# Performance work log

Hardware: AMD Instinct MI355X
Metric: run time of the kernel (lower is better)

Reference implementation:

```python
import jax, jax.numpy as jnp
import numpy as np

N = 20000        # nodes
E = 320000       # edges (avg degree 16)
F_IN = 256       # n_feat
HID = 64         # n_hid (per-head channels, layer 1)
HEADS = 8        # hard-coded n_head in GAT2
NCLS = 64        # n_classes
NEG_SLOPE = 0.2  # PyG GATv2Conv default leaky_relu slope
EPS = 1e-16      # PyG softmax denominator epsilon


def setup_inputs() -> dict:
    key = jax.random.key(0)
    ks = jax.random.split(key, 10)
    glorot = lambda k, shape: jax.random.normal(k, shape, jnp.float32) * (1.0 / np.sqrt(shape[0]))
    return {
        "x": jax.random.normal(ks[0], (N, F_IN), jnp.float32),
        "edge_index": jax.random.randint(ks[1], (2, E), 0, N, dtype=jnp.int32),
        # layer 1: GATv2Conv(F_IN -> HID, heads=HEADS, concat=True)
        "Wl1": glorot(ks[2], (F_IN, HEADS * HID)),
        "Wr1": glorot(ks[3], (F_IN, HEADS * HID)),
        "att1": glorot(ks[4], (HEADS, HID)),
        "b1": jnp.zeros((HEADS * HID,), jnp.float32),
        # layer 2: GATv2Conv(HEADS*HID -> NCLS, heads=1, concat=False)
        "Wl2": glorot(ks[5], (HEADS * HID, NCLS)),
        "Wr2": glorot(ks[6], (HEADS * HID, NCLS)),
        "att2": glorot(ks[7], (1, NCLS)),
        "b2": jnp.zeros((NCLS,), jnp.float32),
    }


def gatv2_layer(x, Wl, Wr, att, bias, src, dst, heads, concat):
    # x: [N, Fin]; Wl/Wr: [Fin, heads*C]; att: [heads, C]
    n = x.shape[0]
    c = att.shape[1]
    xl = (x @ Wl).reshape(n, heads, c)   # source-side projection
    xr = (x @ Wr).reshape(n, heads, c)   # target-side projection
    # per-edge GATv2 score: a^T leaky_relu(Wl x_j + Wr x_i)
    e = jax.nn.leaky_relu(xl[src] + xr[dst], NEG_SLOPE)      # [E, H, C]
    alpha = jnp.einsum('ehc,hc->eh', e, att)                 # [E, H]
    # segment softmax over incoming edges of each target node
    amax = jax.ops.segment_max(alpha, dst, num_segments=n)   # [N, H]
    amax = jnp.where(jnp.isfinite(amax), amax, 0.0)
    ex = jnp.exp(alpha - amax[dst])
    denom = jax.ops.segment_sum(ex, dst, num_segments=n)     # [N, H]
    w = ex / (denom[dst] + EPS)                              # [E, H]
    # weighted scatter-aggregate of source features
    out = jax.ops.segment_sum(xl[src] * w[:, :, None], dst, num_segments=n)  # [N, H, C]
    out = out.reshape(n, heads * c) if concat else out.mean(axis=1)
    return out + bias


def reference(x, edge_index, Wl1, Wr1, att1, b1, Wl2, Wr2, att2, b2):
    src, dst = edge_index[0], edge_index[1]
    h = gatv2_layer(x, Wl1, Wr1, att1, b1, src, dst, HEADS, True)   # [N, 512]
    h = jax.nn.elu(h)
    out = gatv2_layer(h, Wl2, Wr2, att2, b2, src, dst, 1, False)    # [N, 64]
    return out
```

## Files before the change

kernel.cpp:

```cpp
#include <hip/hip_runtime.h>
#include <hip/hip_bf16.h>

#define N_NODES 20000
#define N_EDGES 320000
#define F_IN 256
#define HID 64
#define HEADS 8
#define NCLS 64
#define D1 (HEADS * HID)
#define SCAN_BLOCKS ((N_NODES + 255) / 256)

typedef __attribute__((ext_vector_type(8))) short short8;
typedef __attribute__((ext_vector_type(4))) float floatx4;
typedef __attribute__((ext_vector_type(2))) float v2f;

__device__ __forceinline__ ushort f2bf(float f) {
    unsigned u = __float_as_uint(f);
    unsigned r = (u + 0x7fffu + ((u >> 16) & 1u)) >> 16;
    return (ushort)r;
}
__device__ __forceinline__ v2f unpack2(unsigned u) {
    v2f r;
    r.x = __uint_as_float(u << 16);
    r.y = __uint_as_float(u & 0xffff0000u);
    return r;
}
template <int CTRL>
__device__ __forceinline__ float dppadd(float x) {
    int y = __builtin_amdgcn_update_dpp(0, __float_as_int(x), CTRL, 0xF, 0xF, true);
    return x + __int_as_float(y);
}
__device__ __forceinline__ float rowsum8(float x) {
    x = dppadd<0xB1>(x);
    x = dppadd<0x4E>(x);
    x = dppadd<0x141>(x);
    return x;
}
__device__ __forceinline__ float rowsum16(float x) {
    x = dppadd<0xB1>(x);
    x = dppadd<0x4E>(x);
    x = dppadd<0x124>(x);
    x = dppadd<0x128>(x);
    return x;
}
__device__ __forceinline__ float rowsum32(float x) {
    x = rowsum16(x);
    float t = __int_as_float(__builtin_amdgcn_ds_swizzle(__float_as_int(x), 0x401F));
    return x + t;
}

#define PB_HIST 1250
#define PB_CONV 5000
#define PB_T1   512
#define PB_T2   128
#define PB_TOTAL (PB_HIST + PB_CONV + 2 * PB_T1 + 2 * PB_T2)
__global__ __launch_bounds__(256) void preprocess(
    const float* __restrict__ x, ushort* __restrict__ xbf,
    const float* __restrict__ Wl1, const float* __restrict__ Wr1,
    const float* __restrict__ Wl2, const float* __restrict__ Wr2,
    ushort* __restrict__ wt1, ushort* __restrict__ wt2,
    const int* __restrict__ dst, int* __restrict__ cnt) {
    int b = blockIdx.x, t = threadIdx.x;
    if (b < PB_HIST) {
        int i = b * 256 + t;
        if (i < N_EDGES) atomicAdd(&cnt[dst[i]], 1);
    } else if (b < PB_HIST + PB_CONV) {
        int i = (b - PB_HIST) * 256 + t;
        if (i < N_NODES * F_IN / 4) {
            float4 v = ((const float4*)x)[i];
            ushort4 o;
            o.x = f2bf(v.x); o.y = f2bf(v.y); o.z = f2bf(v.z); o.w = f2bf(v.w);
            ((ushort4*)xbf)[i] = o;
        }
    } else if (b < PB_HIST + PB_CONV + 2 * PB_T1) {
        int lb = b - PB_HIST - PB_CONV;
        const float* W = (lb < PB_T1) ? Wl1 : Wr1;
        ushort* Wt = wt1 + ((lb < PB_T1) ? 0 : D1 * F_IN);
        int i = (lb % PB_T1) * 256 + t;
        if (i < D1 * F_IN) {
            int n = i >> 8, k = i & 255;
            Wt[i] = f2bf(W[(size_t)k * D1 + n]);
        }
    } else {
        int lb = b - PB_HIST - PB_CONV - 2 * PB_T1;
        const float* W = (lb < PB_T2) ? Wl2 : Wr2;
        ushort* Wt = wt2 + ((lb < PB_T2) ? 0 : NCLS * D1);
        int i = (lb % PB_T2) * 256 + t;
        if (i < NCLS * D1) {
            int n = i >> 9, k = i & 511;
            Wt[i] = f2bf(W[(size_t)k * NCLS + n]);
        }
    }
}

__global__ __launch_bounds__(256) void scan_local(const int* __restrict__ cnt,
                                                  int* __restrict__ pscan,
                                                  int* __restrict__ bsum, int n) {
    int tid = threadIdx.x;
    int i = blockIdx.x * 256 + tid;
    int lane = tid & 63, wave = tid >> 6;
    int v = (i < n) ? cnt[i] : 0;
    int x = v;
    #pragma unroll
    for (int d = 1; d < 64; d <<= 1) {
        int y = __shfl_up(x, d);
        if (lane >= d) x += y;
    }
    __shared__ int wsum[4];
    if (lane == 63) wsum[wave] = x;
    __syncthreads();
    int woff = 0;
    for (int w2 = 0; w2 < wave; w2++) woff += wsum[w2];
    int incl = x + woff;
    if (i < n) pscan[i] = incl;
    if (tid == 255) bsum[blockIdx.x] = incl;
}

__global__ __launch_bounds__(256) void scan_finalize(const int* __restrict__ cnt,
                                                     const int* __restrict__ pscan,
                                                     const int* __restrict__ bsum,
                                                     int* __restrict__ row_ptr,
                                                     int* __restrict__ cursor, int n) {
    int t = threadIdx.x;
    int lane = t & 63, wave = t >> 6;
    int v = (t < SCAN_BLOCKS && t < blockIdx.x) ? bsum[t] : 0;
    #pragma unroll
    for (int mask = 1; mask < 64; mask <<= 1) v += __shfl_xor(v, mask);
    __shared__ int ws[4];
    __shared__ int soff;
    if (lane == 0) ws[wave] = v;
    __syncthreads();
    if (t == 0) soff = ws[0] + ws[1] + ws[2] + ws[3];
    __syncthreads();
    int i = blockIdx.x * 256 + t;
    if (i < n) {
        int incl = pscan[i] + soff;
        row_ptr[i + 1] = incl;
        cursor[i] = incl - cnt[i];
    }
    if (i == 0) row_ptr[0] = 0;
}

#define APAD 40
#define G1_NT 8
#define G1_MT ((N_NODES + 127) / 128)
#define G1_BLOCKS (G1_NT * G1_MT)
#define SC_BLOCKS (N_EDGES / 256)
__global__ __launch_bounds__(256) void gemm1_scatter(
    const ushort* __restrict__ A, const ushort* __restrict__ Bt,
    ushort* __restrict__ C,
    const int* __restrict__ src, const int* __restrict__ dst,
    int* __restrict__ cursor, int* __restrict__ csr_src) {
    if (blockIdx.x >= G1_BLOCKS) {
        int i = (blockIdx.x - G1_BLOCKS) * 256 + threadIdx.x;
        if (i < N_EDGES) {
            int d = dst[i];
            int pos = atomicAdd(&cursor[d], 1);
            csr_src[pos] = src[i];
        }
        return;
    }
    const int M = N_NODES, N = 2 * D1, K = F_IN;
    __shared__ ushort As[128 * APAD];
    __shared__ ushort Bs[128 * APAD];
    int tid = threadIdx.x;
    int rowBase = (blockIdx.x >> 3) * 128, colBase = (blockIdx.x & 7) * 128;
    int wave = tid >> 6, lane = tid & 63;
    int quad = lane >> 4, m16 = lane & 15;
    int rh = wave >> 1, chf = wave & 1;
    floatx4 acc[4][4];
    #pragma unroll
    for (int i = 0; i < 4; i++)
        #pragma unroll
        for (int j = 0; j < 4; j++) acc[i][j] = (floatx4){0.f, 0.f, 0.f, 0.f};

    for (int k0 = 0; k0 < K; k0 += 32) {
        #pragma unroll
        for (int i = 0; i < 2; i++) {
            int idx = i * 256 + tid;
            int r = idx >> 2, kq = (idx & 3) * 8;
            int grow = rowBase + r;
            uint4 v = make_uint4(0, 0, 0, 0);
            if (grow < M) v = *(const uint4*)(A + (size_t)grow * K + k0 + kq);
            *(uint4*)&As[r * APAD + kq] = v;
            uint4 w = *(const uint4*)(Bt + (size_t)(colBase + r) * K + k0 + kq);
            *(uint4*)&Bs[r * APAD + kq] = w;
        }
        __syncthreads();
        short8 af[4], bfr[4];
        #pragma unroll
        for (int i = 0; i < 4; i++)
            af[i] = *(short8*)&As[(rh * 64 + i * 16 + m16) * APAD + quad * 8];
        #pragma unroll
        for (int j = 0; j < 4; j++)
            bfr[j] = *(short8*)&Bs[(chf * 64 + j * 16 + m16) * APAD + quad * 8];
        #pragma unroll
        for (int i = 0; i < 4; i++)
            #pragma unroll
            for (int j = 0; j < 4; j++)
                acc[i][j] = __builtin_amdgcn_mfma_f32_16x16x32_bf16(af[i], bfr[j], acc[i][j], 0, 0, 0);
        __syncthreads();
    }
    #pragma unroll
    for (int i = 0; i < 4; i++)
        #pragma unroll
        for (int j = 0; j < 4; j++)
            #pragma unroll
            for (int r = 0; r < 4; r++) {
                int row = rowBase + rh * 64 + i * 16 + quad * 4 + r;
                if (row < M) C[(size_t)row * N + colBase + chf * 64 + j * 16 + m16] = f2bf(acc[i][j][r]);
            }
}

__global__ __launch_bounds__(256) void gemm2_32x128(
    const ushort* __restrict__ A, const ushort* __restrict__ Bt,
    ushort* __restrict__ C) {
    const int K = D1;
    __shared__ ushort As[32 * APAD];
    __shared__ ushort Bs[128 * APAD];
    int tid = threadIdx.x;
    int rowBase = blockIdx.x * 32;
    int wave = tid >> 6, lane = tid & 63;
    int quad = lane >> 4, m16 = lane & 15;
    floatx4 acc[2][2];
    #pragma unroll
    for (int i = 0; i < 2; i++)
        #pragma unroll
        for (int j = 0; j < 2; j++) acc[i][j] = (floatx4){0.f, 0.f, 0.f, 0.f};

    for (int k0 = 0; k0 < K; k0 += 32) {
        if (tid < 128) {
            int r = tid >> 2, kq = (tid & 3) * 8;
            uint4 v = *(const uint4*)(A + (size_t)(rowBase + r) * K + k0 + kq);
            *(uint4*)&As[r * APAD + kq] = v;
        }
        #pragma unroll
        for (int i = 0; i < 2; i++) {
            int idx = i * 256 + tid;
            int r = idx >> 2, kq = (idx & 3) * 8;
            uint4 v = *(const uint4*)(Bt + (size_t)r * K + k0 + kq);
            *(uint4*)&Bs[r * APAD + kq] = v;
        }
        __syncthreads();
        short8 af[2], bfr[2];
        #pragma unroll
        for (int i = 0; i < 2; i++)
            af[i] = *(short8*)&As[(i * 16 + m16) * APAD + quad * 8];
        #pragma unroll
        for (int j = 0; j < 2; j++)
            bfr[j] = *(short8*)&Bs[(wave * 32 + j * 16 + m16) * APAD + quad * 8];
        #pragma unroll
        for (int i = 0; i < 2; i++)
            #pragma unroll
            for (int j = 0; j < 2; j++)
                acc[i][j] = __builtin_amdgcn_mfma_f32_16x16x32_bf16(af[i], bfr[j], acc[i][j], 0, 0, 0);
        __syncthreads();
    }
    #pragma unroll
    for (int i = 0; i < 2; i++)
        #pragma unroll
        for (int j = 0; j < 2; j++)
            #pragma unroll
            for (int r = 0; r < 4; r++) {
                int row = rowBase + i * 16 + quad * 4 + r;
                C[(size_t)row * 128 + wave * 32 + j * 16 + m16] = f2bf(acc[i][j][r]);
            }
}

#define L1PROC(cu, valid)                                                     \
    {                                                                         \
        v2f _c01 = unpack2((cu).x), _c23 = unpack2((cu).y);                   \
        v2f _c45 = unpack2((cu).z), _c67 = unpack2((cu).w);                   \
        v2f _v01 = _c01 + xr01, _v23 = _c23 + xr23;                           \
        v2f _v45 = _c45 + xr45, _v67 = _c67 + xr67;                           \
        v2f _sp = a6_01 * _v01 + a4_01 * __builtin_elementwise_abs(_v01);     \
        _sp = _sp + a6_23 * _v23 + a4_23 * __builtin_elementwise_abs(_v23);   \
        _sp = _sp + a6_45 * _v45 + a4_45 * __builtin_elementwise_abs(_v45);   \
        _sp = _sp + a6_67 * _v67 + a4_67 * __builtin_elementwise_abs(_v67);   \
        float _sc = _sp.x + _sp.y;                                            \
        _sc = rowsum8(_sc);                                                   \
        float _e = (valid) ? exp2f(_sc) : 0.f;                                \
        den += _e;                                                            \
        v2f _ev = {_e, _e};                                                   \
        ac01 = ac01 + _ev * _c01; ac23 = ac23 + _ev * _c23;                   \
        ac45 = ac45 + _ev * _c45; ac67 = ac67 + _ev * _c67;                   \
    }

__global__ __launch_bounds__(128) void attn_l1_fused(
    const ushort* __restrict__ xlr, const float* __restrict__ att,
    const float* __restrict__ b1,
    const int* __restrict__ row_ptr, const int* __restrict__ csr_src,
    ushort* __restrict__ h1out) {
    int d = blockIdx.x;
    int wave = threadIdx.x >> 6, lane = threadIdx.x & 63;
    int start = row_ptr[d], deg = row_ptr[d + 1] - start;

    uint4 xru = *(const uint4*)(xlr + (size_t)d * 1024 + 512 + 8 * lane);
    v2f xr01 = unpack2(xru.x), xr23 = unpack2(xru.y);
    v2f xr45 = unpack2(xru.z), xr67 = unpack2(xru.w);
    const float C6 = 0.6f * 1.44269504f, C4 = 0.4f * 1.44269504f;
    float4 atA = *(const float4*)(att + 8 * lane);
    float4 atB = *(const float4*)(att + 8 * lane + 4);
    v2f a6_01 = {C6 * atA.x, C6 * atA.y}, a4_01 = {C4 * atA.x, C4 * atA.y};
    v2f a6_23 = {C6 * atA.z, C6 * atA.w}, a4_23 = {C4 * atA.z, C4 * atA.w};
    v2f a6_45 = {C6 * atB.x, C6 * atB.y}, a4_45 = {C4 * atB.x, C4 * atB.y};
    v2f a6_67 = {C6 * atB.z, C6 * atB.w}, a4_67 = {C4 * atB.z, C4 * atB.w};

    float den = 0.f;
    v2f ac01 = {0.f, 0.f}, ac23 = {0.f, 0.f}, ac45 = {0.f, 0.f}, ac67 = {0.f, 0.f};

    int S = (deg > wave) ? ((deg - wave + 1) >> 1) : 0;
    if (S > 0) {
        const int* cs = csr_src + start + wave;
        uint4 q0 = *(const uint4*)(xlr + (size_t)cs[0] * 1024 + 8 * lane);
        uint4 q1 = *(const uint4*)(xlr + (size_t)cs[2 * min(1, S - 1)] * 1024 + 8 * lane);
        uint4 q2 = *(const uint4*)(xlr + (size_t)cs[2 * min(2, S - 1)] * 1024 + 8 * lane);
        uint4 q3 = *(const uint4*)(xlr + (size_t)cs[2 * min(3, S - 1)] * 1024 + 8 * lane);
        for (int i0 = 0; i0 < S; i0 += 4) {
            uint4 e0 = q0, e1 = q1, e2 = q2, e3 = q3;
            if (i0 + 4 < S) q0 = *(const uint4*)(xlr + (size_t)cs[2 * (i0 + 4)] * 1024 + 8 * lane);
            if (i0 + 5 < S) q1 = *(const uint4*)(xlr + (size_t)cs[2 * (i0 + 5)] * 1024 + 8 * lane);
            if (i0 + 6 < S) q2 = *(const uint4*)(xlr + (size_t)cs[2 * (i0 + 6)] * 1024 + 8 * lane);
            if (i0 + 7 < S) q3 = *(const uint4*)(xlr + (size_t)cs[2 * (i0 + 7)] * 1024 + 8 * lane);
            L1PROC(e0, true)
            L1PROC(e1, i0 + 1 < S)
            L1PROC(e2, i0 + 2 < S)
            L1PROC(e3, i0 + 3 < S)
        }
    }
    __shared__ float sden2[64];
    __shared__ float sacc[64][10];
    if (wave == 1) {
        sden2[lane] = den;
        float4 f0 = {ac01.x, ac01.y, ac23.x, ac23.y};
        float4 f1 = {ac45.x, ac45.y, ac67.x, ac67.y};
        *(float4*)&sacc[lane][0] = f0;
        *(float4*)&sacc[lane][4] = f1;
    }
    __syncthreads();
    if (wave == 0) {
        den += sden2[lane];
        float4 g0 = *(float4*)&sacc[lane][0];
        float4 g1 = *(float4*)&sacc[lane][4];
        float inv = 1.f / (den + 1e-16f);
        float4 bA = *(const float4*)(b1 + 8 * lane);
        float4 bB = *(const float4*)(b1 + 8 * lane + 4);
        float o0 = (ac01.x + g0.x) * inv + bA.x;
        float o1 = (ac01.y + g0.y) * inv + bA.y;
        float o2 = (ac23.x + g0.z) * inv + bA.z;
        float o3 = (ac23.y + g0.w) * inv + bA.w;
        float o4 = (ac45.x + g1.x) * inv + bB.x;
        float o5 = (ac45.y + g1.y) * inv + bB.y;
        float o6 = (ac67.x + g1.z) * inv + bB.z;
        float o7 = (ac67.y + g1.w) * inv + bB.w;
        o0 = o0 > 0.f ? o0 : (__expf(o0) - 1.f);
        o1 = o1 > 0.f ? o1 : (__expf(o1) - 1.f);
        o2 = o2 > 0.f ? o2 : (__expf(o2) - 1.f);
        o3 = o3 > 0.f ? o3 : (__expf(o3) - 1.f);
        o4 = o4 > 0.f ? o4 : (__expf(o4) - 1.f);
        o5 = o5 > 0.f ? o5 : (__expf(o5) - 1.f);
        o6 = o6 > 0.f ? o6 : (__expf(o6) - 1.f);
        o7 = o7 > 0.f ? o7 : (__expf(o7) - 1.f);
        ushort4 h0, h1v;
        h0.x = f2bf(o0); h0.y = f2bf(o1); h0.z = f2bf(o2); h0.w = f2bf(o3);
        h1v.x = f2bf(o4); h1v.y = f2bf(o5); h1v.z = f2bf(o6); h1v.w = f2bf(o7);
        *(ushort4*)(h1out + (size_t)d * D1 + 8 * lane) = h0;
        *(ushort4*)(h1out + (size_t)d * D1 + 8 * lane + 4) = h1v;
    }
}

#define L2PROC(cu, valid)                                                     \
    {                                                                         \
        v2f _cv = unpack2(cu);                                                \
        v2f _vv = _cv + yr2;                                                  \
        v2f _spv = at6 * _vv + at4 * __builtin_elementwise_abs(_vv);          \
        float _sc = _spv.x + _spv.y;                                          \
        _sc = rowsum32(_sc);                                                  \
        float _e = (valid) ? exp2f(_sc) : 0.f;                                \
        den += _e;                                                            \
        v2f _ev = {_e, _e};                                                   \
        acc = acc + _ev * _cv;                                                \
    }

__global__ __launch_bounds__(256) void attn_l2_fused(
    const ushort* __restrict__ ylr, const float* __restrict__ att2,
    const float* __restrict__ b2,
    const int* __restrict__ row_ptr, const int* __restrict__ csr_src,
    float* __restrict__ out) {
    int wave = threadIdx.x >> 6, lane = threadIdx.x & 63;
    int d = blockIdx.x * 4 + wave;
    if (d >= N_NODES) return;
    int half = lane >> 5, l31 = lane & 31;
    int start = row_ptr[d], deg = row_ptr[d + 1] - start;

    unsigned yru = *(const unsigned*)(ylr + (size_t)d * 128 + 64 + 2 * l31);
    v2f yr2 = unpack2(yru);
    float2 a2 = *(const float2*)(att2 + 2 * l31);
    const float C6 = 0.6f * 1.44269504f, C4 = 0.4f * 1.44269504f;
    v2f at6 = {C6 * a2.x, C6 * a2.y};
    v2f at4 = {C4 * a2.x, C4 * a2.y};

    float den = 0.f;
    v2f acc = {0.f, 0.f};

    if (deg > 0) {
        int S = (deg + 1) >> 1;
        const int* cs = csr_src + start;
        int p0i = min(0 + half, deg - 1);
        int p1i = min(2 * min(1, S - 1) + half, deg - 1);
        int p2i = min(2 * min(2, S - 1) + half, deg - 1);
        int p3i = min(2 * min(3, S - 1) + half, deg - 1);
        unsigned y0 = *(const unsigned*)(ylr + (size_t)cs[p0i] * 128 + 2 * l31);
        unsigned y1 = *(const unsigned*)(ylr + (size_t)cs[p1i] * 128 + 2 * l31);
        unsigned y2 = *(const unsigned*)(ylr + (size_t)cs[p2i] * 128 + 2 * l31);
        unsigned y3 = *(const unsigned*)(ylr + (size_t)cs[p3i] * 128 + 2 * l31);
        for (int i0 = 0; i0 < S; i0 += 4) {
            unsigned u0 = y0, u1 = y1, u2 = y2, u3 = y3;
            if (i0 + 4 < S) { int p = min(2 * (i0 + 4) + half, deg - 1); y0 = *(const unsigned*)(ylr + (size_t)cs[p] * 128 + 2 * l31); }
            if (i0 + 5 < S) { int p = min(2 * (i0 + 5) + half, deg - 1); y1 = *(const unsigned*)(ylr + (size_t)cs[p] * 128 + 2 * l31); }
            if (i0 + 6 < S) { int p = min(2 * (i0 + 6) + half, deg - 1); y2 = *(const unsigned*)(ylr + (size_t)cs[p] * 128 + 2 * l31); }
            if (i0 + 7 < S) { int p = min(2 * (i0 + 7) + half, deg - 1); y3 = *(const unsigned*)(ylr + (size_t)cs[p] * 128 + 2 * l31); }
            L2PROC(u0, 2 * (i0 + 0) + half < deg)
            L2PROC(u1, 2 * (i0 + 1) + half < deg)
            L2PROC(u2, 2 * (i0 + 2) + half < deg)
            L2PROC(u3, 2 * (i0 + 3) + half < deg)
        }
        den += __shfl_xor(den, 32);
        acc.x += __shfl_xor(acc.x, 32);
        acc.y += __shfl_xor(acc.y, 32);
    }
    if (half == 0) {
        float inv = 1.f / (den + 1e-16f);
        float2 bv = *(const float2*)(b2 + 2 * l31);
        float2 o;
        o.x = acc.x * inv + bv.x;
        o.y = acc.y * inv + bv.y;
        *(float2*)(out + (size_t)d * NCLS + 2 * l31) = o;
    }
}

extern "C" void kernel_launch(void* const* d_in, const int* in_sizes, int n_in,
                              void* d_out, int out_size, void* d_ws, size_t ws_size,
                              hipStream_t stream) {
    const float* x    = (const float*)d_in[0];
    const int*   edge = (const int*)d_in[1];
    const float* Wl1  = (const float*)d_in[2];
    const float* Wr1  = (const float*)d_in[3];
    const float* att1 = (const float*)d_in[4];
    const float* b1   = (const float*)d_in[5];
    const float* Wl2  = (const float*)d_in[6];
    const float* Wr2  = (const float*)d_in[7];
    const float* att2 = (const float*)d_in[8];
    const float* b2   = (const float*)d_in[9];
    float* out = (float*)d_out;

    const int* srcv = edge;
    const int* dstv = edge + N_EDGES;

    ushort* xbf  = (ushort*)d_ws;
    ushort* wt1  = xbf + (size_t)N_NODES * F_IN;
    ushort* wt2  = wt1 + 2 * D1 * F_IN;
    ushort* xlr  = wt2 + 2 * NCLS * D1;
    ushort* h1   = xlr + (size_t)N_NODES * 2 * D1;
    ushort* ylr  = h1 + (size_t)N_NODES * D1;
    int* cnt     = (int*)(ylr + (size_t)N_NODES * 2 * NCLS);
    int* pscan   = cnt + N_NODES;
    int* bsum    = pscan + N_NODES;
    int* row_ptr = bsum + 128;
    int* cursor  = row_ptr + N_NODES + 1;
    int* csr_src = cursor + N_NODES;

    hipMemsetAsync(cnt, 0, N_NODES * sizeof(int), stream);
    preprocess<<<PB_TOTAL, 256, 0, stream>>>(x, xbf, Wl1, Wr1, Wl2, Wr2, wt1, wt2, dstv, cnt);
    scan_local<<<SCAN_BLOCKS, 256, 0, stream>>>(cnt, pscan, bsum, N_NODES);
    scan_finalize<<<SCAN_BLOCKS, 256, 0, stream>>>(cnt, pscan, bsum, row_ptr, cursor, N_NODES);
    gemm1_scatter<<<G1_BLOCKS + SC_BLOCKS, 256, 0, stream>>>(
        xbf, wt1, xlr, srcv, dstv, cursor, csr_src);
    attn_l1_fused<<<N_NODES, 128, 0, stream>>>(xlr, att1, b1, row_ptr, csr_src, h1);
    gemm2_32x128<<<N_NODES / 32, 256, 0, stream>>>(h1, wt2, ylr);
    attn_l2_fused<<<(N_NODES + 3) / 4, 256, 0, stream>>>(ylr, att2, b2, row_ptr, csr_src, out);
}
```

Baseline: 227.1 us.

## Use async global-to-LDS loads in GEMMs and remap attention work per wave

Both GEMMs now stage tiles with global_load_lds direct-to-LDS copies into an unpadded 32-wide layout, replacing register round-trips and the padded layout. Layer-1 attention assigns one wave per node, removing the two-wave edge split and its LDS reduction and barrier. Layer-2 attention processes four edges per wave in 16-lane groups with 4 channels per lane, ending in a cross-group reduction. The trade-offs are possible LDS bank conflicts from dropping padding, and less memory-level parallelism per node in layer 1.

```diff
diff --git a/kernel.cpp b/kernel.cpp
--- a/kernel.cpp
+++ b/kernel.cpp
@@ -43,10 +43,10 @@
     x = dppadd<0x128>(x);
     return x;
 }
-__device__ __forceinline__ float rowsum32(float x) {
-    x = rowsum16(x);
-    float t = __int_as_float(__builtin_amdgcn_ds_swizzle(__float_as_int(x), 0x401F));
-    return x + t;
+__device__ __forceinline__ void async_copy16(ushort* lds, const ushort* g) {
+    __builtin_amdgcn_global_load_lds(
+        (const __attribute__((address_space(1))) void*)g,
+        (__attribute__((address_space(3))) void*)lds, 16, 0, 0);
 }
 
 #define PB_HIST 1250
@@ -141,7 +141,6 @@
     if (i == 0) row_ptr[0] = 0;
 }
 
-#define APAD 40
 #define G1_NT 8
 #define G1_MT ((N_NODES + 127) / 128)
 #define G1_BLOCKS (G1_NT * G1_MT)
@@ -161,8 +160,8 @@
         return;
     }
     const int M = N_NODES, N = 2 * D1, K = F_IN;
-    __shared__ ushort As[128 * APAD];
-    __shared__ ushort Bs[128 * APAD];
+    __shared__ ushort As[128 * 32];
+    __shared__ ushort Bs[128 * 32];
     int tid = threadIdx.x;
     int rowBase = (blockIdx.x >> 3) * 128, colBase = (blockIdx.x & 7) * 128;
     int wave = tid >> 6, lane = tid & 63;
@@ -179,21 +178,18 @@
         for (int i = 0; i < 2; i++) {
             int idx = i * 256 + tid;
             int r = idx >> 2, kq = (idx & 3) * 8;
-            int grow = rowBase + r;
-            uint4 v = make_uint4(0, 0, 0, 0);
-            if (grow < M) v = *(const uint4*)(A + (size_t)grow * K + k0 + kq);
-            *(uint4*)&As[r * APAD + kq] = v;
-            uint4 w = *(const uint4*)(Bt + (size_t)(colBase + r) * K + k0 + kq);
-            *(uint4*)&Bs[r * APAD + kq] = w;
+            int grow = min(rowBase + r, M - 1);
+            async_copy16(&As[idx * 8], A + (size_t)grow * K + k0 + kq);
+            async_copy16(&Bs[idx * 8], Bt + (size_t)(colBase + r) * K + k0 + kq);
         }
         __syncthreads();
         short8 af[4], bfr[4];
         #pragma unroll
         for (int i = 0; i < 4; i++)
-            af[i] = *(short8*)&As[(rh * 64 + i * 16 + m16) * APAD + quad * 8];
+            af[i] = *(short8*)&As[(rh * 64 + i * 16 + m16) * 32 + quad * 8];
         #pragma unroll
         for (int j = 0; j < 4; j++)
-            bfr[j] = *(short8*)&Bs[(chf * 64 + j * 16 + m16) * APAD + quad * 8];
+            bfr[j] = *(short8*)&Bs[(chf * 64 + j * 16 + m16) * 32 + quad * 8];
         #pragma unroll
         for (int i = 0; i < 4; i++)
             #pragma unroll
@@ -216,8 +212,8 @@
     const ushort* __restrict__ A, const ushort* __restrict__ Bt,
     ushort* __restrict__ C) {
     const int K = D1;
-    __shared__ ushort As[32 * APAD];
-    __shared__ ushort Bs[128 * APAD];
+    __shared__ ushort As[32 * 32];
+    __shared__ ushort Bs[128 * 32];
     int tid = threadIdx.x;
     int rowBase = blockIdx.x * 32;
     int wave = tid >> 6, lane = tid & 63;
@@ -231,24 +227,22 @@
     for (int k0 = 0; k0 < K; k0 += 32) {
         if (tid < 128) {
             int r = tid >> 2, kq = (tid & 3) * 8;
-            uint4 v = *(const uint4*)(A + (size_t)(rowBase + r) * K + k0 + kq);
-            *(uint4*)&As[r * APAD + kq] = v;
+            async_copy16(&As[tid * 8], A + (size_t)(rowBase + r) * K + k0 + kq);
         }
         #pragma unroll
         for (int i = 0; i < 2; i++) {
             int idx = i * 256 + tid;
             int r = idx >> 2, kq = (idx & 3) * 8;
-            uint4 v = *(const uint4*)(Bt + (size_t)r * K + k0 + kq);
-            *(uint4*)&Bs[r * APAD + kq] = v;
+            async_copy16(&Bs[idx * 8], Bt + (size_t)r * K + k0 + kq);
         }
         __syncthreads();
         short8 af[2], bfr[2];
         #pragma unroll
         for (int i = 0; i < 2; i++)
-            af[i] = *(short8*)&As[(i * 16 + m16) * APAD + quad * 8];
+            af[i] = *(short8*)&As[(i * 16 + m16) * 32 + quad * 8];
         #pragma unroll
         for (int j = 0; j < 2; j++)
-            bfr[j] = *(short8*)&Bs[(wave * 32 + j * 16 + m16) * APAD + quad * 8];
+            bfr[j] = *(short8*)&Bs[(wave * 32 + j * 16 + m16) * 32 + quad * 8];
         #pragma unroll
         for (int i = 0; i < 2; i++)
             #pragma unroll
@@ -286,13 +280,13 @@
         ac45 = ac45 + _ev * _c45; ac67 = ac67 + _ev * _c67;                   \
     }
 
-__global__ __launch_bounds__(128) void attn_l1_fused(
+__global__ __launch_bounds__(256) void attn_l1_fused(
     const ushort* __restrict__ xlr, const float* __restrict__ att,
     const float* __restrict__ b1,
     const int* __restrict__ row_ptr, const int* __restrict__ csr_src,
     ushort* __restrict__ h1out) {
-    int d = blockIdx.x;
     int wave = threadIdx.x >> 6, lane = threadIdx.x & 63;
+    int d = blockIdx.x * 4 + wave;
     int start = row_ptr[d], deg = row_ptr[d + 1] - start;
 
     uint4 xru = *(const uint4*)(xlr + (size_t)d * 1024 + 512 + 8 * lane);
@@ -309,78 +303,70 @@
     float den = 0.f;
     v2f ac01 = {0.f, 0.f}, ac23 = {0.f, 0.f}, ac45 = {0.f, 0.f}, ac67 = {0.f, 0.f};
 
-    int S = (deg > wave) ? ((deg - wave + 1) >> 1) : 0;
-    if (S > 0) {
-        const int* cs = csr_src + start + wave;
+    if (deg > 0) {
+        const int* cs = csr_src + start;
         uint4 q0 = *(const uint4*)(xlr + (size_t)cs[0] * 1024 + 8 * lane);
-        uint4 q1 = *(const uint4*)(xlr + (size_t)cs[2 * min(1, S - 1)] * 1024 + 8 * lane);
-        uint4 q2 = *(const uint4*)(xlr + (size_t)cs[2 * min(2, S - 1)] * 1024 + 8 * lane);
-        uint4 q3 = *(const uint4*)(xlr + (size_t)cs[2 * min(3, S - 1)] * 1024 + 8 * lane);
-        for (int i0 = 0; i0 < S; i0 += 4) {
+        uint4 q1 = *(const uint4*)(xlr + (size_t)cs[min(1, deg - 1)] * 1024 + 8 * lane);
+        uint4 q2 = *(const uint4*)(xlr + (size_t)cs[min(2, deg - 1)] * 1024 + 8 * lane);
+        uint4 q3 = *(const uint4*)(xlr + (size_t)cs[min(3, deg - 1)] * 1024 + 8 * lane);
+        for (int i0 = 0; i0 < deg; i0 += 4) {
             uint4 e0 = q0, e1 = q1, e2 = q2, e3 = q3;
-            if (i0 + 4 < S) q0 = *(const uint4*)(xlr + (size_t)cs[2 * (i0 + 4)] * 1024 + 8 * lane);
-            if (i0 + 5 < S) q1 = *(const uint4*)(xlr + (size_t)cs[2 * (i0 + 5)] * 1024 + 8 * lane);
-            if (i0 + 6 < S) q2 = *(const uint4*)(xlr + (size_t)cs[2 * (i0 + 6)] * 1024 + 8 * lane);
-            if (i0 + 7 < S) q3 = *(const uint4*)(xlr + (size_t)cs[2 * (i0 + 7)] * 1024 + 8 * lane);
+            if (i0 + 4 < deg) q0 = *(const uint4*)(xlr + (size_t)cs[i0 + 4] * 1024 + 8 * lane);
+            if (i0 + 5 < deg) q1 = *(const uint4*)(xlr + (size_t)cs[i0 + 5] * 1024 + 8 * lane);
+            if (i0 + 6 < deg) q2 = *(const uint4*)(xlr + (size_t)cs[i0 + 6] * 1024 + 8 * lane);
+            if (i0 + 7 < deg) q3 = *(const uint4*)(xlr + (size_t)cs[i0 + 7] * 1024 + 8 * lane);
             L1PROC(e0, true)
-            L1PROC(e1, i0 + 1 < S)
-            L1PROC(e2, i0 + 2 < S)
-            L1PROC(e3, i0 + 3 < S)
-        }
-    }
-    __shared__ float sden2[64];
-    __shared__ float sacc[64][10];
-    if (wave == 1) {
-        sden2[lane] = den;
-        float4 f0 = {ac01.x, ac01.y, ac23.x, ac23.y};
-        float4 f1 = {ac45.x, ac45.y, ac67.x, ac67.y};
-        *(float4*)&sacc[lane][0] = f0;
-        *(float4*)&sacc[lane][4] = f1;
-    }
-    __syncthreads();
-    if (wave == 0) {
-        den += sden2[lane];
-        float4 g0 = *(float4*)&sacc[lane][0];
-        float4 g1 = *(float4*)&sacc[lane][4];
-        float inv = 1.f / (den + 1e-16f);
-        float4 bA = *(const float4*)(b1 + 8 * lane);
-        float4 bB = *(const float4*)(b1 + 8 * lane + 4);
-        float o0 = (ac01.x + g0.x) * inv + bA.x;
-        float o1 = (ac01.y + g0.y) * inv + bA.y;
-        float o2 = (ac23.x + g0.z) * inv + bA.z;
-        float o3 = (ac23.y + g0.w) * inv + bA.w;
-        float o4 = (ac45.x + g1.x) * inv + bB.x;
-        float o5 = (ac45.y + g1.y) * inv + bB.y;
-        float o6 = (ac67.x + g1.z) * inv + bB.z;
-        float o7 = (ac67.y + g1.w) * inv + bB.w;
-        o0 = o0 > 0.f ? o0 : (__expf(o0) - 1.f);
-        o1 = o1 > 0.f ? o1 : (__expf(o1) - 1.f);
-        o2 = o2 > 0.f ? o2 : (__expf(o2) - 1.f);
-        o3 = o3 > 0.f ? o3 : (__expf(o3) - 1.f);
-        o4 = o4 > 0.f ? o4 : (__expf(o4) - 1.f);
-        o5 = o5 > 0.f ? o5 : (__expf(o5) - 1.f);
-        o6 = o6 > 0.f ? o6 : (__expf(o6) - 1.f);
-        o7 = o7 > 0.f ? o7 : (__expf(o7) - 1.f);
-        ushort4 h0, h1v;
-        h0.x = f2bf(o0); h0.y = f2bf(o1); h0.z = f2bf(o2); h0.w = f2bf(o3);
-        h1v.x = f2bf(o4); h1v.y = f2bf(o5); h1v.z = f2bf(o6); h1v.w = f2bf(o7);
-        *(ushort4*)(h1out + (size_t)d * D1 + 8 * lane) = h0;
-        *(ushort4*)(h1out + (size_t)d * D1 + 8 * lane + 4) = h1v;
-    }
+            L1PROC(e1, i0 + 1 < deg)
+            L1PROC(e2, i0 + 2 < deg)
+            L1PROC(e3, i0 + 3 < deg)
+        }
+    }
+    float inv = 1.f / (den + 1e-16f);
+    float4 bA = *(const float4*)(b1 + 8 * lane);
+    float4 bB = *(const float4*)(b1 + 8 * lane + 4);
+    float o0 = ac01.x * inv + bA.x;
+    float o1 = ac01.y * inv + bA.y;
+    float o2 = ac23.x * inv + bA.z;
+    float o3 = ac23.y * inv + bA.w;
+    float o4 = ac45.x * inv + bB.x;
+    float o5 = ac45.y * inv + bB.y;
+    float o6 = ac67.x * inv + bB.z;
+    float o7 = ac67.y * inv + bB.w;
+    o0 = o0 > 0.f ? o0 : (__expf(o0) - 1.f);
+    o1 = o1 > 0.f ? o1 : (__expf(o1) - 1.f);
+    o2 = o2 > 0.f ? o2 : (__expf(o2) - 1.f);
+    o3 = o3 > 0.f ? o3 : (__expf(o3) - 1.f);
+    o4 = o4 > 0.f ? o4 : (__expf(o4) - 1.f);
+    o5 = o5 > 0.f ? o5 : (__expf(o5) - 1.f);
+    o6 = o6 > 0.f ? o6 : (__expf(o6) - 1.f);
+    o7 = o7 > 0.f ? o7 : (__expf(o7) - 1.f);
+    ushort4 h0, h1v;
+    h0.x = f2bf(o0); h0.y = f2bf(o1); h0.z = f2bf(o2); h0.w = f2bf(o3);
+    h1v.x = f2bf(o4); h1v.y = f2bf(o5); h1v.z = f2bf(o6); h1v.w = f2bf(o7);
+    *(ushort4*)(h1out + (size_t)d * D1 + 8 * lane) = h0;
+    *(ushort4*)(h1out + (size_t)d * D1 + 8 * lane + 4) = h1v;
 }
 
 #define L2PROC(cu, valid)                                                     \
     {                                                                         \
-        v2f _cv = unpack2(cu);                                                \
-        v2f _vv = _cv + yr2;                                                  \
-        v2f _spv = at6 * _vv + at4 * __builtin_elementwise_abs(_vv);          \
-        float _sc = _spv.x + _spv.y;                                          \
-        _sc = rowsum32(_sc);                                                  \
+        v2f _c01 = unpack2((cu).x), _c23 = unpack2((cu).y);                   \
+        v2f _v01 = _c01 + yr01, _v23 = _c23 + yr23;                           \
+        v2f _sp = at6_01 * _v01 + at4_01 * __builtin_elementwise_abs(_v01)    \
+                + at6_23 * _v23 + at4_23 * __builtin_elementwise_abs(_v23);   \
+        float _sc = _sp.x + _sp.y;                                            \
+        _sc = rowsum16(_sc);                                                  \
         float _e = (valid) ? exp2f(_sc) : 0.f;                                \
         den += _e;                                                            \
         v2f _ev = {_e, _e};                                                   \
-        acc = acc + _ev * _cv;                                                \
-    }
+        ac01 = ac01 + _ev * _c01; ac23 = ac23 + _ev * _c23;                   \
+    }
+
+__device__ __forceinline__ float xgroup_sum(float x) {
+    float t = __int_as_float(__builtin_amdgcn_ds_swizzle(__float_as_int(x), 0x401F));
+    x += t;
+    x += __shfl_xor(x, 32);
+    return x;
+}
 
 __global__ __launch_bounds__(256) void attn_l2_fused(
     const ushort* __restrict__ ylr, const float* __restrict__ att2,
@@ -389,53 +375,48 @@
     float* __restrict__ out) {
     int wave = threadIdx.x >> 6, lane = threadIdx.x & 63;
     int d = blockIdx.x * 4 + wave;
-    if (d >= N_NODES) return;
-    int half = lane >> 5, l31 = lane & 31;
+    int grp = lane >> 4, l15 = lane & 15;
     int start = row_ptr[d], deg = row_ptr[d + 1] - start;
 
-    unsigned yru = *(const unsigned*)(ylr + (size_t)d * 128 + 64 + 2 * l31);
-    v2f yr2 = unpack2(yru);
-    float2 a2 = *(const float2*)(att2 + 2 * l31);
+    uint2 yru = *(const uint2*)(ylr + (size_t)d * 128 + 64 + 4 * l15);
+    v2f yr01 = unpack2(yru.x), yr23 = unpack2(yru.y);
+    float4 a2 = *(const float4*)(att2 + 4 * l15);
     const float C6 = 0.6f * 1.44269504f, C4 = 0.4f * 1.44269504f;
-    v2f at6 = {C6 * a2.x, C6 * a2.y};
-    v2f at4 = {C4 * a2.x, C4 * a2.y};
+    v2f at6_01 = {C6 * a2.x, C6 * a2.y}, at4_01 = {C4 * a2.x, C4 * a2.y};
+    v2f at6_23 = {C6 * a2.z, C6 * a2.w}, at4_23 = {C4 * a2.z, C4 * a2.w};
 
     float den = 0.f;
-    v2f acc = {0.f, 0.f};
+    v2f ac01 = {0.f, 0.f}, ac23 = {0.f, 0.f};
 
     if (deg > 0) {
-        int S = (deg + 1) >> 1;
+        int S = (deg + 3) >> 2;
         const int* cs = csr_src + start;
-        int p0i = min(0 + half, deg - 1);
-        int p1i = min(2 * min(1, S - 1) + half, deg - 1);
-        int p2i = min(2 * min(2, S - 1) + half, deg - 1);
-        int p3i = min(2 * min(3, S - 1) + half, deg - 1);
-        unsigned y0 = *(const unsigned*)(ylr + (size_t)cs[p0i] * 128 + 2 * l31);
-        unsigned y1 = *(const unsigned*)(ylr + (size_t)cs[p1i] * 128 + 2 * l31);
-        unsigned y2 = *(const unsigned*)(ylr + (size_t)cs[p2i] * 128 + 2 * l31);
-        unsigned y3 = *(const unsigned*)(ylr + (size_t)cs[p3i] * 128 + 2 * l31);
-        for (int i0 = 0; i0 < S; i0 += 4) {
-            unsigned u0 = y0, u1 = y1, u2 = y2, u3 = y3;
-            if (i0 + 4 < S) { int p = min(2 * (i0 + 4) + half, deg - 1); y0 = *(const unsigned*)(ylr + (size_t)cs[p] * 128 + 2 * l31); }
-            if (i0 + 5 < S) { int p = min(2 * (i0 + 5) + half, deg - 1); y1 = *(const unsigned*)(ylr + (size_t)cs[p] * 128 + 2 * l31); }
-            if (i0 + 6 < S) { int p = min(2 * (i0 + 6) + half, deg - 1); y2 = *(const unsigned*)(ylr + (size_t)cs[p] * 128 + 2 * l31); }
-            if (i0 + 7 < S) { int p = min(2 * (i0 + 7) + half, deg - 1); y3 = *(const unsigned*)(ylr + (size_t)cs[p] * 128 + 2 * l31); }
-            L2PROC(u0, 2 * (i0 + 0) + half < deg)
-            L2PROC(u1, 2 * (i0 + 1) + half < deg)
-            L2PROC(u2, 2 * (i0 + 2) + half < deg)
-            L2PROC(u3, 2 * (i0 + 3) + half < deg)
-        }
-        den += __shfl_xor(den, 32);
-        acc.x += __shfl_xor(acc.x, 32);
-        acc.y += __shfl_xor(acc.y, 32);
-    }
-    if (half == 0) {
+        uint2 q0 = *(const uint2*)(ylr + (size_t)cs[min(grp, deg - 1)] * 128 + 4 * l15);
+        uint2 q1 = *(const uint2*)(ylr + (size_t)cs[min(min(1, S - 1) * 4 + grp, deg - 1)] * 128 + 4 * l15);
+        for (int i = 0; i < S; i++) {
+            uint2 cu = q0;
+            q0 = q1;
+            if (i + 2 < S) {
+                int p = min((i + 2) * 4 + grp, deg - 1);
+                q1 = *(const uint2*)(ylr + (size_t)cs[p] * 128 + 4 * l15);
+            }
+            L2PROC(cu, 4 * i + grp < deg)
+        }
+        den = xgroup_sum(den);
+        ac01.x = xgroup_sum(ac01.x);
+        ac01.y = xgroup_sum(ac01.y);
+        ac23.x = xgroup_sum(ac23.x);
+        ac23.y = xgroup_sum(ac23.y);
+    }
+    if (grp == 0) {
         float inv = 1.f / (den + 1e-16f);
-        float2 bv = *(const float2*)(b2 + 2 * l31);
-        float2 o;
-        o.x = acc.x * inv + bv.x;
-        o.y = acc.y * inv + bv.y;
-        *(float2*)(out + (size_t)d * NCLS + 2 * l31) = o;
+        float4 bv = *(const float4*)(b2 + 4 * l15);
+        float4 o;
+        o.x = ac01.x * inv + bv.x;
+        o.y = ac01.y * inv + bv.y;
+        o.z = ac23.x * inv + bv.z;
+        o.w = ac23.y * inv + bv.w;
+        *(float4*)(out + (size_t)d * NCLS + 4 * l15) = o;
     }
 }
 
@@ -476,7 +457,7 @@
     scan_finalize<<<SCAN_BLOCKS, 256, 0, stream>>>(cnt, pscan, bsum, row_ptr, cursor, N_NODES);
     gemm1_scatter<<<G1_BLOCKS + SC_BLOCKS, 256, 0, stream>>>(
         xbf, wt1, xlr, srcv, dstv, cursor, csr_src);
-    attn_l1_fused<<<N_NODES, 128, 0, stream>>>(xlr, att1, b1, row_ptr, csr_src, h1);
+    attn_l1_fused<<<N_NODES / 4, 256, 0, stream>>>(xlr, att1, b1, row_ptr, csr_src, h1);
     gemm2_32x128<<<N_NODES / 32, 256, 0, stream>>>(h1, wt2, ylr);
-    attn_l2_fused<<<(N_NODES + 3) / 4, 256, 0, stream>>>(ylr, att2, b2, row_ptr, csr_src, out);
-}
+    attn_l2_fused<<<N_NODES / 4, 256, 0, stream>>>(ylr, att2, b2, row_ptr, csr_src, out);
+}
```

Measured after the change: 223.3 us. No clear change (-1.7%).
